# Optimization experiments

Hardware: AMD Instinct MI355X
Metric: run time of the kernel (lower is better)

## Reference

```python
import jax, jax.numpy as jnp
import numpy as np

B, S, D_IN, D_OUT, RANK = 4, 2048, 4096, 4096, 16
SCALING = 32.0 / RANK  # alpha / rank
MASK_DENSITY = 0.01


def setup_inputs() -> dict:
    key = jax.random.key(0)
    ks = jax.random.split(key, 7)
    x = jax.random.normal(ks[0], (B, S, D_IN), dtype=jnp.float32)
    W = jax.random.normal(ks[1], (D_OUT, D_IN), dtype=jnp.float32) / np.sqrt(D_IN)
    b = jax.random.normal(ks[2], (D_OUT,), dtype=jnp.float32) * 0.01
    lora_A = jax.random.normal(ks[3], (RANK, D_IN), dtype=jnp.float32) / np.sqrt(D_IN)
    lora_B = jax.random.normal(ks[4], (D_OUT, RANK), dtype=jnp.float32) * 0.01
    delta = jax.random.normal(ks[5], (D_OUT, D_IN), dtype=jnp.float32) * 0.01
    mask = jax.random.bernoulli(ks[6], MASK_DENSITY, (D_OUT, D_IN))
    return {"x": x, "W": W, "b": b, "lora_A": lora_A, "lora_B": lora_B,
            "delta": delta, "mask": mask}


def reference(x, W, b, lora_A, lora_B, delta, mask):
    # frozen linear: [B,S,D_in] @ [D_in,D_out] + b
    out = jnp.einsum("bsd,od->bso", x, W) + b
    # LoRA branch: (x @ A^T) @ B^T * scaling
    out = out + jnp.einsum("bsr,or->bso", jnp.einsum("bsd,rd->bsr", x, lora_A), lora_B) * SCALING
    # sparse delta branch: F.linear(x, delta * mask)
    masked_delta = delta * mask.astype(delta.dtype)
    out = out + jnp.einsum("bsd,od->bso", x, masked_delta)
    return out
```

## Files before the change

kernel.cpp:

```cpp
#include <hip/hip_runtime.h>
#include <hip/hip_bf16.h>

typedef __hip_bfloat16 bf16;
typedef __attribute__((ext_vector_type(8))) short bf16x8;
typedef __attribute__((ext_vector_type(4))) float f32x4;
typedef __attribute__((ext_vector_type(4))) int int4v;

#define AS1 __attribute__((address_space(1)))
#define AS3 __attribute__((address_space(3)))

#define MDIM 8192
#define NDIM 4096
#define KDIM 4096
#define SCALING 2.0f

__global__ __launch_bounds__(256) void fold_weff(
    const float* __restrict__ W, const float* __restrict__ lA,
    const float* __restrict__ lB, const float* __restrict__ delta,
    const int* __restrict__ mask, bf16* __restrict__ Weff)
{
    int idx = blockIdx.x * 256 + threadIdx.x;
    int o   = idx >> 9;
    int d0  = (idx & 511) << 3;
    size_t base = (size_t)o * KDIM + d0;

    float Bo[16];
#pragma unroll
    for (int r = 0; r < 16; ++r) Bo[r] = lB[o * 16 + r];

    f32x4 wa = *(const f32x4*)(W + base);
    f32x4 wb = *(const f32x4*)(W + base + 4);
    f32x4 da = *(const f32x4*)(delta + base);
    f32x4 db = *(const f32x4*)(delta + base + 4);

    int mk[8];
    *(int4v*)(mk)     = *(const int4v*)(mask + base);
    *(int4v*)(mk + 4) = *(const int4v*)(mask + base + 4);

    float lor[8] = {0.f, 0.f, 0.f, 0.f, 0.f, 0.f, 0.f, 0.f};
#pragma unroll
    for (int r = 0; r < 16; ++r) {
        f32x4 aa = *(const f32x4*)(lA + (size_t)r * KDIM + d0);
        f32x4 ab = *(const f32x4*)(lA + (size_t)r * KDIM + d0 + 4);
#pragma unroll
        for (int e = 0; e < 4; ++e) {
            lor[e]     += Bo[r] * aa[e];
            lor[e + 4] += Bo[r] * ab[e];
        }
    }

    int4v ov4;
    bf16* ov = (bf16*)&ov4;
#pragma unroll
    for (int e = 0; e < 8; ++e) {
        float w = (e < 4) ? wa[e] : wb[e - 4];
        float d = (e < 4) ? da[e] : db[e - 4];
        float a = w + SCALING * lor[e];
        if (mk[e]) a += d;
        ov[e] = __float2bfloat16(a);
    }
    *(int4v*)(Weff + base) = ov4;
}

__global__ __launch_bounds__(256) void convert_x(
    const float* __restrict__ X, bf16* __restrict__ Xb)
{
    size_t i = ((size_t)blockIdx.x * 256 + threadIdx.x) * 8;
    f32x4 a = *(const f32x4*)(X + i);
    f32x4 b = *(const f32x4*)(X + i + 4);
    int4v ov4;
    bf16* ov = (bf16*)&ov4;
#pragma unroll
    for (int e = 0; e < 4; ++e) {
        ov[e]     = __float2bfloat16(a[e]);
        ov[e + 4] = __float2bfloat16(b[e]);
    }
    *(int4v*)(Xb + i) = ov4;
}

__global__ __launch_bounds__(256, 4) void gemm_bf16(
    const bf16* __restrict__ X, const bf16* __restrict__ Wt,
    const float* __restrict__ bias, float* __restrict__ out)
{
    __shared__ bf16 As[128 * 64];
    __shared__ bf16 Bs[128 * 64];

    const int tid  = threadIdx.x;
    const int lane = tid & 63;
    const int wave = tid >> 6;
    const int wm   = wave & 1;
    const int wn   = wave >> 1;
    const int quad = lane >> 4;
    const int l16  = lane & 15;

    const int bn = blockIdx.x * 128;
    const int bm = blockIdx.y * 128;
    const int cwave = tid & ~63;

    f32x4 acc[4][4];
#pragma unroll
    for (int i = 0; i < 4; ++i)
#pragma unroll
        for (int j = 0; j < 4; ++j)
            acc[i][j] = (f32x4){0.f, 0.f, 0.f, 0.f};

    for (int kt = 0; kt < KDIM / 64; ++kt) {
        const int k0 = kt * 64;
        if (kt) __syncthreads();
#pragma unroll
        for (int j = 0; j < 4; ++j) {
            const int c  = j * 256 + tid;
            const int m  = c >> 3;
            const int kc = (c & 7) ^ (m & 7);
            const int cb = j * 256 + cwave;
            __builtin_amdgcn_global_load_lds(
                (const AS1 void*)(X + (size_t)(bm + m) * KDIM + k0 + kc * 8),
                (AS3 void*)(As + cb * 8), 16, 0, 0);
            __builtin_amdgcn_global_load_lds(
                (const AS1 void*)(Wt + (size_t)(bn + m) * KDIM + k0 + kc * 8),
                (AS3 void*)(Bs + cb * 8), 16, 0, 0);
        }
        __syncthreads();

#pragma unroll
        for (int ks = 0; ks < 2; ++ks) {
            bf16x8 af[4], bfr[4];
#pragma unroll
            for (int i = 0; i < 4; ++i) {
                const int m   = wm * 64 + i * 16 + l16;
                const int kca = (ks * 4 + quad) ^ (m & 7);
                af[i] = *(const bf16x8*)(As + m * 64 + kca * 8);
                const int n   = wn * 64 + i * 16 + l16;
                const int kcb = (ks * 4 + quad) ^ (n & 7);
                bfr[i] = *(const bf16x8*)(Bs + n * 64 + kcb * 8);
            }
#pragma unroll
            for (int i = 0; i < 4; ++i)
#pragma unroll
                for (int j = 0; j < 4; ++j)
                    acc[i][j] = __builtin_amdgcn_mfma_f32_16x16x32_bf16(
                        af[i], bfr[j], acc[i][j], 0, 0, 0);
        }
    }

    float bv[4];
#pragma unroll
    for (int j = 0; j < 4; ++j)
        bv[j] = bias[bn + wn * 64 + j * 16 + l16];

#pragma unroll
    for (int i = 0; i < 4; ++i) {
        const int mg = bm + wm * 64 + i * 16 + quad * 4;
#pragma unroll
        for (int j = 0; j < 4; ++j) {
            const int ng = bn + wn * 64 + j * 16 + l16;
#pragma unroll
            for (int r = 0; r < 4; ++r)
                out[(size_t)(mg + r) * NDIM + ng] = acc[i][j][r] + bv[j];
        }
    }
}

__global__ __launch_bounds__(256, 3) void gemm_f32(
    const float* __restrict__ X, const bf16* __restrict__ Wt,
    const float* __restrict__ bias, float* __restrict__ out)
{
    __shared__ float Asf[128 * 64];
    __shared__ bf16  Bs[128 * 64];

    const int tid  = threadIdx.x;
    const int lane = tid & 63;
    const int wave = tid >> 6;
    const int wm   = wave & 1;
    const int wn   = wave >> 1;
    const int quad = lane >> 4;
    const int l16  = lane & 15;

    const int bn = blockIdx.x * 128;
    const int bm = blockIdx.y * 128;
    const int cwave = tid & ~63;

    f32x4 acc[4][4];
#pragma unroll
    for (int i = 0; i < 4; ++i)
#pragma unroll
        for (int j = 0; j < 4; ++j)
            acc[i][j] = (f32x4){0.f, 0.f, 0.f, 0.f};

    for (int kt = 0; kt < KDIM / 64; ++kt) {
        const int k0 = kt * 64;
        if (kt) __syncthreads();
#pragma unroll
        for (int j = 0; j < 8; ++j) {
            const int c  = j * 256 + tid;
            const int m  = c >> 4;
            const int kc = (c & 15) ^ (m & 15);
            const int cb = j * 256 + cwave;
            __builtin_amdgcn_global_load_lds(
                (const AS1 void*)(X + (size_t)(bm + m) * KDIM + k0 + kc * 4),
                (AS3 void*)(Asf + cb * 4), 16, 0, 0);
        }
#pragma unroll
        for (int j = 0; j < 4; ++j) {
            const int c  = j * 256 + tid;
            const int m  = c >> 3;
            const int kc = (c & 7) ^ (m & 7);
            const int cb = j * 256 + cwave;
            __builtin_amdgcn_global_load_lds(
                (const AS1 void*)(Wt + (size_t)(bn + m) * KDIM + k0 + kc * 8),
                (AS3 void*)(Bs + cb * 8), 16, 0, 0);
        }
        __syncthreads();

#pragma unroll
        for (int ks = 0; ks < 2; ++ks) {
            bf16x8 af[4], bfr[4];
#pragma unroll
            for (int i = 0; i < 4; ++i) {
                const int m  = wm * 64 + i * 16 + l16;
                const int k2 = (ks * 4 + quad) * 2;
                f32x4 lo = *(const f32x4*)(Asf + m * 64 + ((k2     ^ (m & 15)) * 4));
                f32x4 hi = *(const f32x4*)(Asf + m * 64 + (((k2+1) ^ (m & 15)) * 4));
                bf16 tmp[8];
#pragma unroll
                for (int e = 0; e < 4; ++e) {
                    tmp[e]     = __float2bfloat16(lo[e]);
                    tmp[e + 4] = __float2bfloat16(hi[e]);
                }
                af[i] = *(const bf16x8*)tmp;

                const int n   = wn * 64 + i * 16 + l16;
                const int kcb = (ks * 4 + quad) ^ (n & 7);
                bfr[i] = *(const bf16x8*)(Bs + n * 64 + kcb * 8);
            }
#pragma unroll
            for (int i = 0; i < 4; ++i)
#pragma unroll
                for (int j = 0; j < 4; ++j)
                    acc[i][j] = __builtin_amdgcn_mfma_f32_16x16x32_bf16(
                        af[i], bfr[j], acc[i][j], 0, 0, 0);
        }
    }

    float bv[4];
#pragma unroll
    for (int j = 0; j < 4; ++j)
        bv[j] = bias[bn + wn * 64 + j * 16 + l16];

#pragma unroll
    for (int i = 0; i < 4; ++i) {
        const int mg = bm + wm * 64 + i * 16 + quad * 4;
#pragma unroll
        for (int j = 0; j < 4; ++j) {
            const int ng = bn + wn * 64 + j * 16 + l16;
#pragma unroll
            for (int r = 0; r < 4; ++r)
                out[(size_t)(mg + r) * NDIM + ng] = acc[i][j][r] + bv[j];
        }
    }
}

extern "C" void kernel_launch(void* const* d_in, const int* in_sizes, int n_in,
                              void* d_out, int out_size, void* d_ws, size_t ws_size,
                              hipStream_t stream)
{
    const float* x     = (const float*)d_in[0];
    const float* W     = (const float*)d_in[1];
    const float* b     = (const float*)d_in[2];
    const float* lA    = (const float*)d_in[3];
    const float* lB    = (const float*)d_in[4];
    const float* delta = (const float*)d_in[5];
    const int*   mask  = (const int*)d_in[6];
    float* out = (float*)d_out;

    bf16* Weff = (bf16*)d_ws;
    bf16* Xb   = (bf16*)((char*)d_ws + (size_t)NDIM * KDIM * 2);

    const size_t need = (size_t)NDIM * KDIM * 2 + (size_t)MDIM * KDIM * 2;

    fold_weff<<<dim3((NDIM * KDIM / 8) / 256), 256, 0, stream>>>(
        W, lA, lB, delta, mask, Weff);

    if (ws_size >= need) {
        convert_x<<<dim3((MDIM * KDIM / 8) / 256), 256, 0, stream>>>(x, Xb);
        gemm_bf16<<<dim3(NDIM / 128, MDIM / 128), 256, 0, stream>>>(
            Xb, Weff, b, out);
    } else {
        gemm_f32<<<dim3(NDIM / 128, MDIM / 128), 256, 0, stream>>>(
            x, Weff, b, out);
    }
}
```

Before: 656.4 us.

## Use 256x256 double-buffered bf16 GEMM with interleaved staging and merge prep kernels

After: 678.0 us. 3.3% more time.

```diff
diff --git a/kernel.cpp b/kernel.cpp
--- a/kernel.cpp
+++ b/kernel.cpp
@@ -13,134 +13,179 @@
 #define NDIM 4096
 #define KDIM 4096
 #define SCALING 2.0f
-
-__global__ __launch_bounds__(256) void fold_weff(
+#define NT (KDIM / 64)
+
+__global__ __launch_bounds__(256) void prep(
     const float* __restrict__ W, const float* __restrict__ lA,
     const float* __restrict__ lB, const float* __restrict__ delta,
-    const int* __restrict__ mask, bf16* __restrict__ Weff)
-{
-    int idx = blockIdx.x * 256 + threadIdx.x;
-    int o   = idx >> 9;
-    int d0  = (idx & 511) << 3;
-    size_t base = (size_t)o * KDIM + d0;
-
-    float Bo[16];
-#pragma unroll
-    for (int r = 0; r < 16; ++r) Bo[r] = lB[o * 16 + r];
-
-    f32x4 wa = *(const f32x4*)(W + base);
-    f32x4 wb = *(const f32x4*)(W + base + 4);
-    f32x4 da = *(const f32x4*)(delta + base);
-    f32x4 db = *(const f32x4*)(delta + base + 4);
-
-    int mk[8];
-    *(int4v*)(mk)     = *(const int4v*)(mask + base);
-    *(int4v*)(mk + 4) = *(const int4v*)(mask + base + 4);
-
-    float lor[8] = {0.f, 0.f, 0.f, 0.f, 0.f, 0.f, 0.f, 0.f};
-#pragma unroll
-    for (int r = 0; r < 16; ++r) {
-        f32x4 aa = *(const f32x4*)(lA + (size_t)r * KDIM + d0);
-        f32x4 ab = *(const f32x4*)(lA + (size_t)r * KDIM + d0 + 4);
+    const int* __restrict__ mask, bf16* __restrict__ Weff,
+    const float* __restrict__ X, bf16* __restrict__ Xb)
+{
+    const int bid = blockIdx.x;
+    if (bid < 8192) {
+        int idx = bid * 256 + threadIdx.x;
+        int o   = idx >> 9;
+        int d0  = (idx & 511) << 3;
+        size_t base = (size_t)o * KDIM + d0;
+
+        float Bo[16];
+#pragma unroll
+        for (int r = 0; r < 16; ++r) Bo[r] = lB[o * 16 + r];
+
+        f32x4 wa = *(const f32x4*)(W + base);
+        f32x4 wb = *(const f32x4*)(W + base + 4);
+        f32x4 da = *(const f32x4*)(delta + base);
+        f32x4 db = *(const f32x4*)(delta + base + 4);
+
+        int mk[8];
+        *(int4v*)(mk)     = *(const int4v*)(mask + base);
+        *(int4v*)(mk + 4) = *(const int4v*)(mask + base + 4);
+
+        float lor[8] = {0.f, 0.f, 0.f, 0.f, 0.f, 0.f, 0.f, 0.f};
+#pragma unroll
+        for (int r = 0; r < 16; ++r) {
+            f32x4 aa = *(const f32x4*)(lA + (size_t)r * KDIM + d0);
+            f32x4 ab = *(const f32x4*)(lA + (size_t)r * KDIM + d0 + 4);
+#pragma unroll
+            for (int e = 0; e < 4; ++e) {
+                lor[e]     += Bo[r] * aa[e];
+                lor[e + 4] += Bo[r] * ab[e];
+            }
+        }
+
+        int4v ov4;
+        bf16* ov = (bf16*)&ov4;
+#pragma unroll
+        for (int e = 0; e < 8; ++e) {
+            float w = (e < 4) ? wa[e] : wb[e - 4];
+            float d = (e < 4) ? da[e] : db[e - 4];
+            float a = w + SCALING * lor[e];
+            if (mk[e]) a += d;
+            ov[e] = __float2bfloat16(a);
+        }
+        *(int4v*)(Weff + base) = ov4;
+    } else {
+        size_t i = ((size_t)(bid - 8192) * 256 + threadIdx.x) * 8;
+        f32x4 a = *(const f32x4*)(X + i);
+        f32x4 b = *(const f32x4*)(X + i + 4);
+        int4v ov4;
+        bf16* ov = (bf16*)&ov4;
 #pragma unroll
         for (int e = 0; e < 4; ++e) {
-            lor[e]     += Bo[r] * aa[e];
-            lor[e + 4] += Bo[r] * ab[e];
-        }
-    }
-
-    int4v ov4;
-    bf16* ov = (bf16*)&ov4;
-#pragma unroll
-    for (int e = 0; e < 8; ++e) {
-        float w = (e < 4) ? wa[e] : wb[e - 4];
-        float d = (e < 4) ? da[e] : db[e - 4];
-        float a = w + SCALING * lor[e];
-        if (mk[e]) a += d;
-        ov[e] = __float2bfloat16(a);
-    }
-    *(int4v*)(Weff + base) = ov4;
-}
-
-__global__ __launch_bounds__(256) void convert_x(
-    const float* __restrict__ X, bf16* __restrict__ Xb)
-{
-    size_t i = ((size_t)blockIdx.x * 256 + threadIdx.x) * 8;
-    f32x4 a = *(const f32x4*)(X + i);
-    f32x4 b = *(const f32x4*)(X + i + 4);
-    int4v ov4;
-    bf16* ov = (bf16*)&ov4;
-#pragma unroll
-    for (int e = 0; e < 4; ++e) {
-        ov[e]     = __float2bfloat16(a[e]);
-        ov[e + 4] = __float2bfloat16(b[e]);
-    }
-    *(int4v*)(Xb + i) = ov4;
-}
-
-__global__ __launch_bounds__(256, 4) void gemm_bf16(
+            ov[e]     = __float2bfloat16(a[e]);
+            ov[e + 4] = __float2bfloat16(b[e]);
+        }
+        *(int4v*)(Xb + i) = ov4;
+    }
+}
+
+__device__ __forceinline__ void stage_half(
+    const bf16* __restrict__ g, int grow0, bf16* l, int half, int kt,
+    int tid, int wvb)
+{
+    const int k0 = (kt < NT) ? kt * 64 : 0;
+#pragma unroll
+    for (int gi = 0; gi < 2; ++gi) {
+        const int c  = gi * 512 + tid;
+        const int ml = c >> 3;
+        const int kc = (c & 7) ^ (ml & 7);
+        __builtin_amdgcn_global_load_lds(
+            (const AS1 void*)(g + (size_t)(grow0 + half * 128 + ml) * KDIM + k0 + kc * 8),
+            (AS3 void*)(l + half * 8192 + (gi * 512 + wvb) * 8),
+            16, 0, 0);
+    }
+}
+
+#define RD_A(i) { const int m_ = wm * 128 + (i) * 16 + l16;                       \
+    a[i][0] = *(const bf16x8*)(Ac + m_ * 64 + ((quad       ^ (m_ & 7)) * 8));     \
+    a[i][1] = *(const bf16x8*)(Ac + m_ * 64 + (((4 + quad) ^ (m_ & 7)) * 8)); }
+#define RD_B(j) { const int n_ = wn * 64 + (j) * 16 + l16;                        \
+    b[j][0] = *(const bf16x8*)(Bc + n_ * 64 + ((quad       ^ (n_ & 7)) * 8));     \
+    b[j][1] = *(const bf16x8*)(Bc + n_ * 64 + (((4 + quad) ^ (n_ & 7)) * 8)); }
+#define MF2(i, j)                                                                 \
+    acc[i][j] = __builtin_amdgcn_mfma_f32_16x16x32_bf16(a[i][0], b[j][0], acc[i][j], 0, 0, 0); \
+    acc[i][j] = __builtin_amdgcn_mfma_f32_16x16x32_bf16(a[i][1], b[j][1], acc[i][j], 0, 0, 0);
+
+__global__ __launch_bounds__(512, 2) void gemm_bf16_256(
     const bf16* __restrict__ X, const bf16* __restrict__ Wt,
     const float* __restrict__ bias, float* __restrict__ out)
 {
-    __shared__ bf16 As[128 * 64];
-    __shared__ bf16 Bs[128 * 64];
+    __shared__ bf16 As[2][256 * 64];
+    __shared__ bf16 Bs[2][256 * 64];
 
     const int tid  = threadIdx.x;
     const int lane = tid & 63;
+    const int wvb  = tid & ~63;
     const int wave = tid >> 6;
     const int wm   = wave & 1;
     const int wn   = wave >> 1;
     const int quad = lane >> 4;
     const int l16  = lane & 15;
 
-    const int bn = blockIdx.x * 128;
-    const int bm = blockIdx.y * 128;
-    const int cwave = tid & ~63;
-
-    f32x4 acc[4][4];
-#pragma unroll
-    for (int i = 0; i < 4; ++i)
+    int idb = blockIdx.y * gridDim.x + blockIdx.x;
+    idb = (idb & 7) * 64 + (idb >> 3);
+    const int bn = (idb & 15) * 256;
+    const int bm = (idb >> 4) * 256;
+
+    f32x4 acc[8][4];
+#pragma unroll
+    for (int i = 0; i < 8; ++i)
 #pragma unroll
         for (int j = 0; j < 4; ++j)
             acc[i][j] = (f32x4){0.f, 0.f, 0.f, 0.f};
 
-    for (int kt = 0; kt < KDIM / 64; ++kt) {
-        const int k0 = kt * 64;
-        if (kt) __syncthreads();
-#pragma unroll
-        for (int j = 0; j < 4; ++j) {
-            const int c  = j * 256 + tid;
-            const int m  = c >> 3;
-            const int kc = (c & 7) ^ (m & 7);
-            const int cb = j * 256 + cwave;
-            __builtin_amdgcn_global_load_lds(
-                (const AS1 void*)(X + (size_t)(bm + m) * KDIM + k0 + kc * 8),
-                (AS3 void*)(As + cb * 8), 16, 0, 0);
-            __builtin_amdgcn_global_load_lds(
-                (const AS1 void*)(Wt + (size_t)(bn + m) * KDIM + k0 + kc * 8),
-                (AS3 void*)(Bs + cb * 8), 16, 0, 0);
-        }
-        __syncthreads();
-
-#pragma unroll
-        for (int ks = 0; ks < 2; ++ks) {
-            bf16x8 af[4], bfr[4];
-#pragma unroll
-            for (int i = 0; i < 4; ++i) {
-                const int m   = wm * 64 + i * 16 + l16;
-                const int kca = (ks * 4 + quad) ^ (m & 7);
-                af[i] = *(const bf16x8*)(As + m * 64 + kca * 8);
-                const int n   = wn * 64 + i * 16 + l16;
-                const int kcb = (ks * 4 + quad) ^ (n & 7);
-                bfr[i] = *(const bf16x8*)(Bs + n * 64 + kcb * 8);
-            }
-#pragma unroll
-            for (int i = 0; i < 4; ++i)
-#pragma unroll
-                for (int j = 0; j < 4; ++j)
-                    acc[i][j] = __builtin_amdgcn_mfma_f32_16x16x32_bf16(
-                        af[i], bfr[j], acc[i][j], 0, 0, 0);
-        }
+    stage_half(X,  bm, As[0], 0, 0, tid, wvb);
+    stage_half(X,  bm, As[0], 1, 0, tid, wvb);
+    stage_half(Wt, bn, Bs[0], 0, 0, tid, wvb);
+    stage_half(Wt, bn, Bs[0], 1, 0, tid, wvb);
+    stage_half(X,  bm, As[1], 0, 1, tid, wvb);
+    stage_half(X,  bm, As[1], 1, 1, tid, wvb);
+    asm volatile("s_waitcnt vmcnt(4)" ::: "memory");
+    __builtin_amdgcn_s_barrier();
+
+    bf16x8 a[8][2], b[4][2];
+
+    for (int t = 0; t < NT; ++t) {
+        const int cur = t & 1;
+        const bf16* Ac = As[cur];
+        const bf16* Bc = Bs[cur];
+
+        RD_A(0) RD_A(1) RD_A(2) RD_A(3)
+        RD_B(0) RD_B(1)
+        stage_half(Wt, bn, Bs[cur ^ 1], 0, t + 1, tid, wvb);
+        __builtin_amdgcn_s_barrier();
+        __builtin_amdgcn_s_setprio(1);
+        MF2(0,0) MF2(1,0) MF2(2,0) MF2(3,0)
+        MF2(0,1) MF2(1,1) MF2(2,1) MF2(3,1)
+        __builtin_amdgcn_s_setprio(0);
+        __builtin_amdgcn_s_barrier();
+
+        RD_A(4) RD_A(5) RD_A(6) RD_A(7)
+        stage_half(Wt, bn, Bs[cur ^ 1], 1, t + 1, tid, wvb);
+        __builtin_amdgcn_s_barrier();
+        __builtin_amdgcn_s_setprio(1);
+        MF2(4,0) MF2(5,0) MF2(6,0) MF2(7,0)
+        MF2(4,1) MF2(5,1) MF2(6,1) MF2(7,1)
+        __builtin_amdgcn_s_setprio(0);
+        __builtin_amdgcn_s_barrier();
+
+        RD_B(2) RD_B(3)
+        stage_half(X, bm, As[cur], 0, t + 2, tid, wvb);
+        __builtin_amdgcn_s_barrier();
+        __builtin_amdgcn_s_setprio(1);
+        MF2(0,2) MF2(1,2) MF2(2,2) MF2(3,2)
+        MF2(0,3) MF2(1,3) MF2(2,3) MF2(3,3)
+        __builtin_amdgcn_s_setprio(0);
+        __builtin_amdgcn_s_barrier();
+
+        stage_half(X, bm, As[cur], 1, t + 2, tid, wvb);
+        __builtin_amdgcn_s_barrier();
+        __builtin_amdgcn_s_setprio(1);
+        MF2(4,2) MF2(5,2) MF2(6,2) MF2(7,2)
+        MF2(4,3) MF2(5,3) MF2(6,3) MF2(7,3)
+        __builtin_amdgcn_s_setprio(0);
+        asm volatile("s_waitcnt vmcnt(4)" ::: "memory");
+        __builtin_amdgcn_s_barrier();
     }
 
     float bv[4];
@@ -149,8 +194,8 @@
         bv[j] = bias[bn + wn * 64 + j * 16 + l16];
 
 #pragma unroll
-    for (int i = 0; i < 4; ++i) {
-        const int mg = bm + wm * 64 + i * 16 + quad * 4;
+    for (int i = 0; i < 8; ++i) {
+        const int mg = bm + wm * 128 + i * 16 + quad * 4;
 #pragma unroll
         for (int j = 0; j < 4; ++j) {
             const int ng = bn + wn * 64 + j * 16 + l16;
@@ -171,8 +216,8 @@
     const int tid  = threadIdx.x;
     const int lane = tid & 63;
     const int wave = tid >> 6;
-    const int wm   = wave & 1;
-    const int wn   = wave >> 1;
+    const int wmf  = wave & 1;
+    const int wnf  = wave >> 1;
     const int quad = lane >> 4;
     const int l16  = lane & 15;
 
@@ -217,7 +262,7 @@
             bf16x8 af[4], bfr[4];
 #pragma unroll
             for (int i = 0; i < 4; ++i) {
-                const int m  = wm * 64 + i * 16 + l16;
+                const int m  = wmf * 64 + i * 16 + l16;
                 const int k2 = (ks * 4 + quad) * 2;
                 f32x4 lo = *(const f32x4*)(Asf + m * 64 + ((k2     ^ (m & 15)) * 4));
                 f32x4 hi = *(const f32x4*)(Asf + m * 64 + (((k2+1) ^ (m & 15)) * 4));
@@ -229,7 +274,7 @@
                 }
                 af[i] = *(const bf16x8*)tmp;
 
-                const int n   = wn * 64 + i * 16 + l16;
+                const int n   = wnf * 64 + i * 16 + l16;
                 const int kcb = (ks * 4 + quad) ^ (n & 7);
                 bfr[i] = *(const bf16x8*)(Bs + n * 64 + kcb * 8);
             }
@@ -245,14 +290,14 @@
     float bv[4];
 #pragma unroll
     for (int j = 0; j < 4; ++j)
-        bv[j] = bias[bn + wn * 64 + j * 16 + l16];
+        bv[j] = bias[bn + wnf * 64 + j * 16 + l16];
 
 #pragma unroll
     for (int i = 0; i < 4; ++i) {
-        const int mg = bm + wm * 64 + i * 16 + quad * 4;
+        const int mg = bm + wmf * 64 + i * 16 + quad * 4;
 #pragma unroll
         for (int j = 0; j < 4; ++j) {
-            const int ng = bn + wn * 64 + j * 16 + l16;
+            const int ng = bn + wnf * 64 + j * 16 + l16;
 #pragma unroll
             for (int r = 0; r < 4; ++r)
                 out[(size_t)(mg + r) * NDIM + ng] = acc[i][j][r] + bv[j];
@@ -278,14 +323,14 @@
 
     const size_t need = (size_t)NDIM * KDIM * 2 + (size_t)MDIM * KDIM * 2;
 
-    fold_weff<<<dim3((NDIM * KDIM / 8) / 256), 256, 0, stream>>>(
-        W, lA, lB, delta, mask, Weff);
-
     if (ws_size >= need) {
-        convert_x<<<dim3((MDIM * KDIM / 8) / 256), 256, 0, stream>>>(x, Xb);
-        gemm_bf16<<<dim3(NDIM / 128, MDIM / 128), 256, 0, stream>>>(
+        prep<<<dim3(8192 + 16384), 256, 0, stream>>>(
+            W, lA, lB, delta, mask, Weff, x, Xb);
+        gemm_bf16_256<<<dim3(NDIM / 256, MDIM / 256), 512, 0, stream>>>(
             Xb, Weff, b, out);
     } else {
+        prep<<<dim3(8192), 256, 0, stream>>>(
+            W, lA, lB, delta, mask, Weff, x, Xb);
         gemm_f32<<<dim3(NDIM / 128, MDIM / 128), 256, 0, stream>>>(
             x, Weff, b, out);
     }
```

## Fuse weight folding and x conversion into one prep kernel; swizzle GEMM tiles

Applied to the files above, without the earlier changes.

Measured after the change: 666.3 us. About the same (+1.5%).

```diff
diff --git a/kernel.cpp b/kernel.cpp
--- a/kernel.cpp
+++ b/kernel.cpp
@@ -14,68 +14,89 @@
 #define KDIM 4096
 #define SCALING 2.0f
 
-__global__ __launch_bounds__(256) void fold_weff(
+__global__ __launch_bounds__(256) void prep(
     const float* __restrict__ W, const float* __restrict__ lA,
     const float* __restrict__ lB, const float* __restrict__ delta,
-    const int* __restrict__ mask, bf16* __restrict__ Weff)
-{
-    int idx = blockIdx.x * 256 + threadIdx.x;
-    int o   = idx >> 9;
-    int d0  = (idx & 511) << 3;
-    size_t base = (size_t)o * KDIM + d0;
-
-    float Bo[16];
-#pragma unroll
-    for (int r = 0; r < 16; ++r) Bo[r] = lB[o * 16 + r];
-
-    f32x4 wa = *(const f32x4*)(W + base);
-    f32x4 wb = *(const f32x4*)(W + base + 4);
-    f32x4 da = *(const f32x4*)(delta + base);
-    f32x4 db = *(const f32x4*)(delta + base + 4);
-
-    int mk[8];
-    *(int4v*)(mk)     = *(const int4v*)(mask + base);
-    *(int4v*)(mk + 4) = *(const int4v*)(mask + base + 4);
-
-    float lor[8] = {0.f, 0.f, 0.f, 0.f, 0.f, 0.f, 0.f, 0.f};
-#pragma unroll
-    for (int r = 0; r < 16; ++r) {
-        f32x4 aa = *(const f32x4*)(lA + (size_t)r * KDIM + d0);
-        f32x4 ab = *(const f32x4*)(lA + (size_t)r * KDIM + d0 + 4);
-#pragma unroll
-        for (int e = 0; e < 4; ++e) {
-            lor[e]     += Bo[r] * aa[e];
-            lor[e + 4] += Bo[r] * ab[e];
-        }
-    }
-
-    int4v ov4;
-    bf16* ov = (bf16*)&ov4;
-#pragma unroll
-    for (int e = 0; e < 8; ++e) {
-        float w = (e < 4) ? wa[e] : wb[e - 4];
-        float d = (e < 4) ? da[e] : db[e - 4];
-        float a = w + SCALING * lor[e];
-        if (mk[e]) a += d;
-        ov[e] = __float2bfloat16(a);
-    }
-    *(int4v*)(Weff + base) = ov4;
-}
-
-__global__ __launch_bounds__(256) void convert_x(
+    const int* __restrict__ mask, bf16* __restrict__ Weff,
     const float* __restrict__ X, bf16* __restrict__ Xb)
 {
-    size_t i = ((size_t)blockIdx.x * 256 + threadIdx.x) * 8;
-    f32x4 a = *(const f32x4*)(X + i);
-    f32x4 b = *(const f32x4*)(X + i + 4);
-    int4v ov4;
-    bf16* ov = (bf16*)&ov4;
-#pragma unroll
-    for (int e = 0; e < 4; ++e) {
-        ov[e]     = __float2bfloat16(a[e]);
-        ov[e + 4] = __float2bfloat16(b[e]);
-    }
-    *(int4v*)(Xb + i) = ov4;
+    __shared__ float sA[16 * 512];
+    const int bid = blockIdx.x;
+    const int tid = threadIdx.x;
+
+    if (bid < 2048) {
+        const int ob = (bid >> 3) * 16;
+        const int db = (bid & 7) * 512;
+
+#pragma unroll
+        for (int i = tid; i < 2048; i += 256) {
+            const int row = i >> 7;
+            const int qc  = (i & 127) * 4;
+            *(f32x4*)(sA + row * 512 + qc) =
+                *(const f32x4*)(lA + (size_t)row * KDIM + db + qc);
+        }
+        __syncthreads();
+
+        for (int c = tid; c < 1024; c += 256) {
+            const int o_l = c >> 6;
+            const int dc  = (c & 63) * 8;
+            const int o   = ob + o_l;
+            const size_t base = (size_t)o * KDIM + db + dc;
+
+            float Bo[16];
+#pragma unroll
+            for (int r = 0; r < 16; ++r) Bo[r] = lB[o * 16 + r];
+
+            f32x4 wa = *(const f32x4*)(W + base);
+            f32x4 wb = *(const f32x4*)(W + base + 4);
+            f32x4 da = *(const f32x4*)(delta + base);
+            f32x4 db4 = *(const f32x4*)(delta + base + 4);
+
+            int mk[8];
+            *(int4v*)(mk)     = *(const int4v*)(mask + base);
+            *(int4v*)(mk + 4) = *(const int4v*)(mask + base + 4);
+
+            float lor[8] = {0.f, 0.f, 0.f, 0.f, 0.f, 0.f, 0.f, 0.f};
+#pragma unroll
+            for (int r = 0; r < 16; ++r) {
+                f32x4 aa = *(const f32x4*)(sA + r * 512 + dc);
+                f32x4 ab = *(const f32x4*)(sA + r * 512 + dc + 4);
+#pragma unroll
+                for (int e = 0; e < 4; ++e) {
+                    lor[e]     += Bo[r] * aa[e];
+                    lor[e + 4] += Bo[r] * ab[e];
+                }
+            }
+
+            int4v ov4;
+            bf16* ov = (bf16*)&ov4;
+#pragma unroll
+            for (int e = 0; e < 8; ++e) {
+                float w = (e < 4) ? wa[e] : wb[e - 4];
+                float d = (e < 4) ? da[e] : db4[e - 4];
+                float a = w + SCALING * lor[e];
+                if (mk[e]) a += d;
+                ov[e] = __float2bfloat16(a);
+            }
+            *(int4v*)(Weff + base) = ov4;
+        }
+    } else {
+        const size_t nchunk = (size_t)MDIM * KDIM / 8;
+        for (size_t c = (size_t)(bid - 2048) * 256 + tid; c < nchunk;
+             c += (size_t)2048 * 256) {
+            const size_t i = c * 8;
+            f32x4 a = *(const f32x4*)(X + i);
+            f32x4 b = *(const f32x4*)(X + i + 4);
+            int4v ov4;
+            bf16* ov = (bf16*)&ov4;
+#pragma unroll
+            for (int e = 0; e < 4; ++e) {
+                ov[e]     = __float2bfloat16(a[e]);
+                ov[e + 4] = __float2bfloat16(b[e]);
+            }
+            *(int4v*)(Xb + i) = ov4;
+        }
+    }
 }
 
 __global__ __launch_bounds__(256, 4) void gemm_bf16(
@@ -93,8 +114,10 @@
     const int quad = lane >> 4;
     const int l16  = lane & 15;
 
-    const int bn = blockIdx.x * 128;
-    const int bm = blockIdx.y * 128;
+    int flat = blockIdx.y * gridDim.x + blockIdx.x;
+    flat = (flat & 7) * 256 + (flat >> 3);
+    const int bn = (flat & 31) * 128;
+    const int bm = (flat >> 5) * 128;
     const int cwave = tid & ~63;
 
     f32x4 acc[4][4];
@@ -171,8 +194,8 @@
     const int tid  = threadIdx.x;
     const int lane = tid & 63;
     const int wave = tid >> 6;
-    const int wm   = wave & 1;
-    const int wn   = wave >> 1;
+    const int wmf  = wave & 1;
+    const int wnf  = wave >> 1;
     const int quad = lane >> 4;
     const int l16  = lane & 15;
 
@@ -217,7 +240,7 @@
             bf16x8 af[4], bfr[4];
 #pragma unroll
             for (int i = 0; i < 4; ++i) {
-                const int m  = wm * 64 + i * 16 + l16;
+                const int m  = wmf * 64 + i * 16 + l16;
                 const int k2 = (ks * 4 + quad) * 2;
                 f32x4 lo = *(const f32x4*)(Asf + m * 64 + ((k2     ^ (m & 15)) * 4));
                 f32x4 hi = *(const f32x4*)(Asf + m * 64 + (((k2+1) ^ (m & 15)) * 4));
@@ -229,7 +252,7 @@
                 }
                 af[i] = *(const bf16x8*)tmp;
 
-                const int n   = wn * 64 + i * 16 + l16;
+                const int n   = wnf * 64 + i * 16 + l16;
                 const int kcb = (ks * 4 + quad) ^ (n & 7);
                 bfr[i] = *(const bf16x8*)(Bs + n * 64 + kcb * 8);
             }
@@ -245,14 +268,14 @@
     float bv[4];
 #pragma unroll
     for (int j = 0; j < 4; ++j)
-        bv[j] = bias[bn + wn * 64 + j * 16 + l16];
+        bv[j] = bias[bn + wnf * 64 + j * 16 + l16];
 
 #pragma unroll
     for (int i = 0; i < 4; ++i) {
-        const int mg = bm + wm * 64 + i * 16 + quad * 4;
+        const int mg = bm + wmf * 64 + i * 16 + quad * 4;
 #pragma unroll
         for (int j = 0; j < 4; ++j) {
-            const int ng = bn + wn * 64 + j * 16 + l16;
+            const int ng = bn + wnf * 64 + j * 16 + l16;
 #pragma unroll
             for (int r = 0; r < 4; ++r)
                 out[(size_t)(mg + r) * NDIM + ng] = acc[i][j][r] + bv[j];
@@ -278,14 +301,14 @@
 
     const size_t need = (size_t)NDIM * KDIM * 2 + (size_t)MDIM * KDIM * 2;
 
-    fold_weff<<<dim3((NDIM * KDIM / 8) / 256), 256, 0, stream>>>(
-        W, lA, lB, delta, mask, Weff);
-
     if (ws_size >= need) {
-        convert_x<<<dim3((MDIM * KDIM / 8) / 256), 256, 0, stream>>>(x, Xb);
+        prep<<<dim3(4096), 256, 0, stream>>>(
+            W, lA, lB, delta, mask, Weff, x, Xb);
         gemm_bf16<<<dim3(NDIM / 128, MDIM / 128), 256, 0, stream>>>(
             Xb, Weff, b, out);
     } else {
+        prep<<<dim3(2048), 256, 0, stream>>>(
+            W, lA, lB, delta, mask, Weff, x, Xb);
         gemm_f32<<<dim3(NDIM / 128, MDIM / 128), 256, 0, stream>>>(
             x, Weff, b, out);
     }
```
